# Performance work log

Hardware: AMD Instinct MI355X
Metric: run time of the kernel (lower is better)

The kernel has to match this reference:

```python
import jax, jax.numpy as jnp
import numpy as np

DIM = 192
HEADS = 6
WS = 7          # window size
SS = 3          # shift size
MLP_H = int(DIM * 4.0)
EPS_LN = 1e-5


def _static_tables():
    # Swin-v2 log-spaced continuous relative coords table: (1, 2*WS-1, 2*WS-1, 2)
    ch = np.arange(-(WS - 1), WS, dtype=np.float32)
    cw = np.arange(-(WS - 1), WS, dtype=np.float32)
    t = np.stack(np.meshgrid(ch, cw, indexing='ij'), axis=-1)[None]
    t[..., 0] /= (WS - 1)
    t[..., 1] /= (WS - 1)
    t *= 7.0
    t = np.sign(t) * np.log2(np.abs(t) + 1.0) / np.log2(7.0)
    # relative position index: (WS*WS, WS*WS)
    coords = np.stack(np.meshgrid(np.arange(WS), np.arange(WS), indexing='ij'))
    cf = coords.reshape(2, -1)
    rc = (cf[:, :, None] - cf[:, None, :]).transpose(1, 2, 0)
    rc[..., 0] += WS - 1
    rc[..., 1] += WS - 1
    rc[..., 0] *= 2 * WS - 1
    rpi = rc.sum(-1)
    return jnp.asarray(t, jnp.float32), jnp.asarray(rpi, jnp.int32)


def _attn_mask(H, W):
    # shifted-window mask: (nW, N, N) with 0 / -100
    img = np.zeros((H, W), np.float32)
    cnt = 0
    for hs in (slice(0, -WS), slice(-WS, -SS), slice(-SS, None)):
        for ws in (slice(0, -WS), slice(-WS, -SS), slice(-SS, None)):
            img[hs, ws] = cnt
            cnt += 1
    mw = img.reshape(H // WS, WS, W // WS, WS).transpose(0, 2, 1, 3).reshape(-1, WS * WS)
    am = mw[:, None, :] - mw[:, :, None]
    am = np.where(am != 0, -100.0, 0.0).astype(np.float32)
    return jnp.asarray(am)


def _ln(x, w, b):
    m = x.mean(-1, keepdims=True)
    v = ((x - m) ** 2).mean(-1, keepdims=True)
    return (x - m) / jnp.sqrt(v + EPS_LN) * w + b


def setup_inputs() -> dict:
    key = jax.random.key(0)
    ks = jax.random.split(key, 16)
    d = DIM
    inp = {
        'x': jax.random.normal(ks[0], (32, 56, 56, d), jnp.float32),
        'qkv_w': jax.random.normal(ks[1], (3 * d, d), jnp.float32) * (2.0 / d) ** 0.5,
        'qkv_b': jnp.full((3 * d,), 0.01, jnp.float32),
        'proj_w': jax.random.normal(ks[2], (d, d), jnp.float32) * (2.0 / d) ** 0.5,
        'proj_b': jnp.full((d,), 0.01, jnp.float32),
        'logit_scale': jnp.log(10.0 * jnp.ones((HEADS, 1, 1), jnp.float32)),
        'cpb_w1': jax.random.normal(ks[3], (512, 2), jnp.float32) * (2.0 / 2) ** 0.5,
        'cpb_b1': jnp.full((512,), 0.01, jnp.float32),
        'cpb_w2': jax.random.normal(ks[4], (HEADS, 512), jnp.float32) * (2.0 / 512) ** 0.5,
        'norm1_w': jnp.ones((d,), jnp.float32),
        'norm1_b': jnp.zeros((d,), jnp.float32),
        'norm2_w': jnp.ones((d,), jnp.float32),
        'norm2_b': jnp.zeros((d,), jnp.float32),
        'fc1_w': jax.random.normal(ks[5], (MLP_H, d), jnp.float32) * (2.0 / d) ** 0.5,
        'fc1_b': jnp.full((MLP_H,), 0.01, jnp.float32),
        'fc2_w': jax.random.normal(ks[6], (d, MLP_H), jnp.float32) * (2.0 / MLP_H) ** 0.5,
        'fc2_b': jnp.full((d,), 0.01, jnp.float32),
    }
    return inp


def reference(x, qkv_w, qkv_b, proj_w, proj_b, logit_scale, cpb_w1, cpb_b1, cpb_w2,
              norm1_w, norm1_b, norm2_w, norm2_b, fc1_w, fc1_b, fc2_w, fc2_b):
    B, H, W, C = x.shape
    N = WS * WS
    hd = C // HEADS
    table, rpi = _static_tables()
    mask = _attn_mask(H, W)  # (nW, N, N)
    nW = mask.shape[0]

    shortcut = x
    # cyclic shift + window partition: (B*nW, N, C)
    xs = jnp.roll(x, (-SS, -SS), axis=(1, 2))
    xw = xs.reshape(B, H // WS, WS, W // WS, WS, C).transpose(0, 1, 3, 2, 4, 5).reshape(-1, N, C)

    qkv = xw @ qkv_w.T + qkv_b
    qkv = qkv.reshape(-1, N, 3, HEADS, hd).transpose(2, 0, 3, 1, 4)
    q, k, v = qkv[0], qkv[1], qkv[2]  # (B_, H, N, hd)

    qn = q / jnp.clip(jnp.linalg.norm(q, axis=-1, keepdims=True), 1e-12)
    kn = k / jnp.clip(jnp.linalg.norm(k, axis=-1, keepdims=True), 1e-12)
    scale = jnp.exp(jnp.minimum(logit_scale, jnp.log(100.0)))  # (HEADS,1,1)
    attn = jnp.einsum('bhnd,bhmd->bhnm', qn, kn) * scale

    # CPB-MLP relative position bias
    hbt = jax.nn.leaky_relu(table @ cpb_w1.T + cpb_b1, 0.01) @ cpb_w2.T  # (1,13,13,HEADS)
    bias_table = hbt.reshape(-1, HEADS)
    rpb = bias_table[rpi.reshape(-1)].reshape(N, N, HEADS).transpose(2, 0, 1)
    attn = attn + (14.0 * jax.nn.sigmoid(rpb))[None]

    # shifted-window mask + softmax
    attn = attn.reshape(B, nW, HEADS, N, N) + mask[None, :, None]
    attn = jax.nn.softmax(attn.reshape(-1, HEADS, N, N), axis=-1)

    out = jnp.einsum('bhnm,bhmd->bnhd', attn, v).reshape(-1, N, C)
    out = out @ proj_w.T + proj_b

    # window reverse + reverse shift
    out = out.reshape(B, H // WS, W // WS, WS, WS, C).transpose(0, 1, 3, 2, 4, 5).reshape(B, H, W, C)
    out = jnp.roll(out, (SS, SS), axis=(1, 2))

    # post-norm residuals (Swin-v2 style)
    x1 = shortcut + _ln(out, norm1_w, norm1_b)
    mlp = jax.nn.gelu(x1 @ fc1_w.T + fc1_b, approximate=False) @ fc2_w.T + fc2_b
    return x1 + _ln(mlp, norm2_w, norm2_b)
```

## Files before the change

### kernel.cpp

```cpp
#include <hip/hip_runtime.h>
#include <math.h>

#define CDIM 192
#define NHEADS 6
#define HDIM 32
#define WSZ 7
#define NTOK 49
#define SHIFT 3
#define HW 56
#define MLPH 768
#define NTOKENS 100352
#define QKS 576
#define XS 200
#define VTS 72
#define PPS 72
#define LS 196
#define QPS 72
#define AS2 200
#define HS2 200
#define OS2 196

typedef __attribute__((ext_vector_type(8))) short short8;
typedef __attribute__((ext_vector_type(4))) float floatx4;
typedef unsigned short ushort_t;
typedef unsigned int uint_t;

__device__ __forceinline__ ushort_t f2b(float f) {
  uint_t u = __float_as_uint(f);
  u = (u + 0x7FFFu + ((u >> 16) & 1u)) >> 16;
  return (ushort_t)u;
}

__device__ __forceinline__ float gelu_fast(float v) {
  float u2 = 1.5957691f * v * (1.0f + 0.044715f * v * v);
  float s = 1.0f / (1.0f + __expf(-u2));
  return v * s;
}

__global__ void prep_kernel(const float* __restrict__ fc1_w, const float* __restrict__ fc2_w,
                            const float* __restrict__ qkv_w, const float* __restrict__ proj_w,
                            ushort_t* __restrict__ w1b, ushort_t* __restrict__ w2b,
                            ushort_t* __restrict__ qwb, ushort_t* __restrict__ pwb) {
  int i = blockIdx.x * 256 + threadIdx.x;
  if (i < MLPH*CDIM) w1b[i] = f2b(fc1_w[i]);
  else if (i < 2*MLPH*CDIM) w2b[i - MLPH*CDIM] = f2b(fc2_w[i - MLPH*CDIM]);
  else if (i < 2*MLPH*CDIM + 3*CDIM*CDIM) qwb[i - 2*MLPH*CDIM] = f2b(qkv_w[i - 2*MLPH*CDIM]);
  else if (i < 2*MLPH*CDIM + 4*CDIM*CDIM)
    pwb[i - 2*MLPH*CDIM - 3*CDIM*CDIM] = f2b(proj_w[i - 2*MLPH*CDIM - 3*CDIM*CDIM]);
}

__global__ __launch_bounds__(256) void cpb1_kernel(const float* __restrict__ w1,
                                                   const float* __restrict__ b1,
                                                   const float* __restrict__ w2,
                                                   float* __restrict__ bt) {
  int wave = threadIdx.x >> 6, lane = threadIdx.x & 63;
  int e = blockIdx.x * 4 + wave;
  if (e >= 169) return;
  const float inv_log2_7 = 0.35620718710802217f;
  int a = e / 13, b = e % 13;
  float v0 = (float)(a - 6) * (7.0f / 6.0f);
  float v1 = (float)(b - 6) * (7.0f / 6.0f);
  float s0 = (v0 > 0.f) ? 1.f : ((v0 < 0.f) ? -1.f : 0.f);
  float s1 = (v1 > 0.f) ? 1.f : ((v1 < 0.f) ? -1.f : 0.f);
  v0 = s0 * log2f(fabsf(v0) + 1.0f) * inv_log2_7;
  v1 = s1 * log2f(fabsf(v1) + 1.0f) * inv_log2_7;
  float acc[NHEADS];
  #pragma unroll
  for (int h = 0; h < NHEADS; ++h) acc[h] = 0.f;
  #pragma unroll
  for (int j = 0; j < 8; ++j) {
    int k = lane + 64*j;
    float hv = v0 * w1[2*k] + v1 * w1[2*k+1] + b1[k];
    hv = (hv > 0.f) ? hv : 0.01f * hv;
    #pragma unroll
    for (int h = 0; h < NHEADS; ++h) acc[h] += hv * w2[h*512 + k];
  }
  #pragma unroll
  for (int m = 1; m < 64; m <<= 1)
    #pragma unroll
    for (int h = 0; h < NHEADS; ++h) acc[h] += __shfl_xor(acc[h], m, 64);
  if (lane == 0) {
    #pragma unroll
    for (int h = 0; h < NHEADS; ++h) bt[e*NHEADS + h] = acc[h];
  }
}

__global__ void cpb2_kernel(const float* __restrict__ bt, float* __restrict__ abias) {
  int e = blockIdx.x * 256 + threadIdx.x;
  if (e >= NHEADS*NTOK*NTOK) return;
  int h = e / (NTOK*NTOK);
  int r = e % (NTOK*NTOK);
  int i = r / NTOK, j = r % NTOK;
  int idx = (i/7 - j/7 + 6) * 13 + (i%7 - j%7 + 6);
  float v = bt[idx*NHEADS + h];
  abias[e] = 14.0f / (1.0f + __expf(-v));
}

__global__ __launch_bounds__(384) void qkv_kernel(
    const float* __restrict__ x, const ushort_t* __restrict__ qwb,
    const float* __restrict__ qkv_b, ushort_t* __restrict__ qkvg) {
  __shared__ __align__(16) ushort_t s_a[64*AS2];
  int tid = threadIdx.x;
  int lane = tid & 63;
  int h = tid >> 6;
  int l15 = lane & 15, quad = lane >> 4;
  size_t tbase = (size_t)blockIdx.x * 64;

  for (int e = tid; e < 64*48; e += 384) {
    int t = e / 48, cc = (e % 48) * 4;
    float4 v = *(const float4*)(x + (tbase + t)*CDIM + cc);
    uint_t p0 = (uint_t)f2b(v.x) | ((uint_t)f2b(v.y) << 16);
    uint_t p1 = (uint_t)f2b(v.z) | ((uint_t)f2b(v.w) << 16);
    *(uint_t*)&s_a[t*AS2 + cc]     = p0;
    *(uint_t*)&s_a[t*AS2 + cc + 2] = p1;
  }
  __syncthreads();

  floatx4 acc[6][4];
  #pragma unroll
  for (int nt = 0; nt < 6; ++nt)
    #pragma unroll
    for (int mt = 0; mt < 4; ++mt) acc[nt][mt] = (floatx4){0.f,0.f,0.f,0.f};
  #pragma unroll
  for (int kt = 0; kt < 6; ++kt) {
    short8 a[4];
    #pragma unroll
    for (int mt = 0; mt < 4; ++mt)
      a[mt] = *(const short8*)&s_a[(mt*16 + l15)*AS2 + kt*32 + quad*8];
    #pragma unroll
    for (int nt = 0; nt < 6; ++nt) {
      int o = (nt >> 1)*CDIM + h*HDIM + (nt & 1)*16 + l15;
      short8 b = *(const short8*)&qwb[(size_t)o*CDIM + kt*32 + quad*8];
      #pragma unroll
      for (int mt = 0; mt < 4; ++mt)
        acc[nt][mt] = __builtin_amdgcn_mfma_f32_16x16x32_bf16(a[mt], b, acc[nt][mt], 0, 0, 0);
    }
  }
  #pragma unroll
  for (int w2 = 0; w2 < 2; ++w2) {
    float b0 = qkv_b[w2*CDIM + h*HDIM + l15];
    float b1 = qkv_b[w2*CDIM + h*HDIM + 16 + l15];
    #pragma unroll
    for (int mt = 0; mt < 4; ++mt) {
      float vv[2][4], ss[4];
      #pragma unroll
      for (int r = 0; r < 4; ++r) {
        float t0 = acc[w2*2][mt][r] + b0;
        float t1 = acc[w2*2+1][mt][r] + b1;
        vv[0][r] = t0; vv[1][r] = t1;
        ss[r] = t0*t0 + t1*t1;
      }
      #pragma unroll
      for (int m = 1; m < 16; m <<= 1)
        #pragma unroll
        for (int r = 0; r < 4; ++r) ss[r] += __shfl_xor(ss[r], m, 64);
      #pragma unroll
      for (int r = 0; r < 4; ++r) {
        float inv = 1.0f / fmaxf(sqrtf(ss[r]), 1e-12f);
        size_t tok = tbase + mt*16 + quad*4 + r;
        qkvg[tok*QKS + w2*CDIM + h*HDIM + l15]      = f2b(vv[0][r] * inv);
        qkvg[tok*QKS + w2*CDIM + h*HDIM + 16 + l15] = f2b(vv[1][r] * inv);
      }
    }
  }
  {
    float b0 = qkv_b[2*CDIM + h*HDIM + l15];
    float b1 = qkv_b[2*CDIM + h*HDIM + 16 + l15];
    #pragma unroll
    for (int mt = 0; mt < 4; ++mt)
      #pragma unroll
      for (int r = 0; r < 4; ++r) {
        size_t tok = tbase + mt*16 + quad*4 + r;
        qkvg[tok*QKS + 2*CDIM + h*HDIM + l15]      = f2b(acc[4][mt][r] + b0);
        qkvg[tok*QKS + 2*CDIM + h*HDIM + 16 + l15] = f2b(acc[5][mt][r] + b1);
      }
  }
}

__global__ __launch_bounds__(512, 4) void attn_kernel(
    const float* __restrict__ x, const ushort_t* __restrict__ qkvg,
    const ushort_t* __restrict__ pwb, const float* __restrict__ proj_b,
    const float* __restrict__ logit_scale, const float* __restrict__ abias,
    const float* __restrict__ n1w, const float* __restrict__ n1b,
    float* __restrict__ outp) {
  __shared__ __align__(16) ushort_t sm[192*VTS + 128*PPS + 64*XS];
  ushort_t* s_vt = sm;
  ushort_t* s_P  = sm + 192*VTS;
  ushort_t* s_o  = s_P + 128*PPS;
  float*    s_ln = (float*)sm;
  __shared__ float s_mu[NTOK], s_rs[NTOK];
  __shared__ int s_id[64];

  int tid = threadIdx.x;
  int lane = tid & 63;
  int wave = tid >> 6;
  int wm = wave & 3, wh = wave >> 2;
  int l15 = lane & 15, quad = lane >> 4;
  int mrow0 = wm*16 + quad*4;
  int blk = blockIdx.x;
  int bimg = blk >> 6, wh_b = (blk >> 3) & 7, ww_b = blk & 7;
  int rbase = wh_b*WSZ, cbase = ww_b*WSZ;

  int ti_a = wm*16 + l15; ti_a = (ti_a < NTOK) ? ti_a : (NTOK-1);
  int ra = rbase + ti_a/7 + SHIFT; ra -= (ra >= HW) ? HW : 0;
  int ca = cbase + ti_a%7 + SHIFT; ca -= (ca >= HW) ? HW : 0;
  uint_t qrow = (uint_t)((bimg*HW + ra)*HW + ca) * QKS;
  uint_t krow[4];
  #pragma unroll
  for (int nt = 0; nt < 4; ++nt) {
    int tn = nt*16 + l15; tn = (tn < NTOK) ? tn : (NTOK-1);
    int r = rbase + tn/7 + SHIFT; r -= (r >= HW) ? HW : 0;
    int c = cbase + tn%7 + SHIFT; c -= (c >= HW) ? HW : 0;
    krow[nt] = (uint_t)((bimg*HW + r)*HW + c) * QKS + CDIM;
  }
  short8 aq[3];
  #pragma unroll
  for (int hh = 0; hh < 3; ++hh)
    aq[hh] = *(const short8*)&qkvg[(size_t)qrow + (wh*3+hh)*HDIM + quad*8];

  if (tid < NTOK) {
    int r = rbase + tid/7;
    int c = cbase + tid%7;
    int hid = (r < HW-WSZ) ? 0 : ((r < HW-SHIFT) ? 1 : 2);
    int wid = (c < HW-WSZ) ? 0 : ((c < HW-SHIFT) ? 1 : 2);
    s_id[tid] = hid*3 + wid;
  }

  for (int e = tid; e < 32*48; e += 512) {
    int tp = e & 31, dg = e >> 5;
    int t0 = 2*tp, t1 = t0 + 1;
    uint2 va = make_uint2(0u, 0u), vb = make_uint2(0u, 0u);
    if (t0 < NTOK) {
      int r = rbase + t0/7 + SHIFT; r -= (r >= HW) ? HW : 0;
      int c = cbase + t0%7 + SHIFT; c -= (c >= HW) ? HW : 0;
      va = *(const uint2*)&qkvg[((size_t)((bimg*HW + r)*HW + c))*QKS + 2*CDIM + dg*4];
    }
    if (t1 < NTOK) {
      int r = rbase + t1/7 + SHIFT; r -= (r >= HW) ? HW : 0;
      int c = cbase + t1%7 + SHIFT; c -= (c >= HW) ? HW : 0;
      vb = *(const uint2*)&qkvg[((size_t)((bimg*HW + r)*HW + c))*QKS + 2*CDIM + dg*4];
    }
    int d = dg*4;
    *(uint_t*)&s_vt[(d  )*VTS + t0] = (va.x & 0xFFFFu) | (vb.x << 16);
    *(uint_t*)&s_vt[(d+1)*VTS + t0] = (va.x >> 16) | (vb.x & 0xFFFF0000u);
    *(uint_t*)&s_vt[(d+2)*VTS + t0] = (va.y & 0xFFFFu) | (vb.y << 16);
    *(uint_t*)&s_vt[(d+3)*VTS + t0] = (va.y >> 16) | (vb.y & 0xFFFF0000u);
  }
  __syncthreads();

  ushort_t* sPh = s_P + wave*16*PPS;
  for (int hh = 0; hh < 3; ++hh) {
    int h = wh*3 + hh;
    short8 bk[4];
    #pragma unroll
    for (int nt = 0; nt < 4; ++nt)
      bk[nt] = *(const short8*)&qkvg[(size_t)krow[nt] + h*HDIM + quad*8];
    floatx4 sv[4];
    #pragma unroll
    for (int nt = 0; nt < 4; ++nt)
      sv[nt] = __builtin_amdgcn_mfma_f32_16x16x32_bf16(aq[hh], bk[nt], (floatx4){0.f,0.f,0.f,0.f}, 0, 0, 0);
    float sc = __expf(fminf(logit_scale[h], 4.6051702f));
    #pragma unroll
    for (int r = 0; r < 4; ++r) {
      int m_tok = mrow0 + r;
      int mi = (m_tok < NTOK) ? m_tok : (NTOK-1);
      float srow[4];
      float mx = -1e30f;
      #pragma unroll
      for (int nt = 0; nt < 4; ++nt) {
        int n = nt*16 + l15;
        int ni = (n < NTOK) ? n : (NTOK-1);
        float s = sv[nt][r]*sc + abias[(h*NTOK + mi)*NTOK + ni];
        if (s_id[mi] != s_id[ni]) s -= 100.f;
        if (n >= NTOK) s = -1e30f;
        srow[nt] = s;
        mx = fmaxf(mx, s);
      }
      #pragma unroll
      for (int m = 1; m < 16; m <<= 1) mx = fmaxf(mx, __shfl_xor(mx, m, 64));
      float p[4], sum = 0.f;
      #pragma unroll
      for (int nt = 0; nt < 4; ++nt) { p[nt] = __expf(srow[nt] - mx); sum += p[nt]; }
      #pragma unroll
      for (int m = 1; m < 16; m <<= 1) sum += __shfl_xor(sum, m, 64);
      float inv = 1.0f / sum;
      #pragma unroll
      for (int nt = 0; nt < 4; ++nt) {
        int n = nt*16 + l15;
        sPh[(quad*4 + r)*PPS + n] = (n < NTOK) ? f2b(p[nt]*inv) : (ushort_t)0;
      }
    }
    floatx4 ov[2];
    ov[0] = (floatx4){0.f,0.f,0.f,0.f}; ov[1] = (floatx4){0.f,0.f,0.f,0.f};
    #pragma unroll
    for (int kt = 0; kt < 2; ++kt) {
      short8 ap = *(const short8*)&sPh[l15*PPS + kt*32 + quad*8];
      #pragma unroll
      for (int dt = 0; dt < 2; ++dt) {
        short8 bv = *(const short8*)&s_vt[(h*HDIM + dt*16 + l15)*VTS + kt*32 + quad*8];
        ov[dt] = __builtin_amdgcn_mfma_f32_16x16x32_bf16(ap, bv, ov[dt], 0, 0, 0);
      }
    }
    #pragma unroll
    for (int dt = 0; dt < 2; ++dt)
      #pragma unroll
      for (int r = 0; r < 4; ++r)
        s_o[(mrow0 + r)*XS + h*HDIM + dt*16 + l15] = f2b(ov[dt][r]);
  }
  __syncthreads();

  short8 aof[6];
  #pragma unroll
  for (int kt = 0; kt < 6; ++kt)
    aof[kt] = *(const short8*)&s_o[(wm*16 + l15)*XS + kt*32 + quad*8];
  floatx4 pacc[6];
  #pragma unroll
  for (int j = 0; j < 6; ++j) pacc[j] = (floatx4){0.f,0.f,0.f,0.f};
  #pragma unroll
  for (int kt = 0; kt < 6; ++kt) {
    #pragma unroll
    for (int j = 0; j < 6; ++j) {
      int n = wh*96 + j*16 + l15;
      short8 b = *(const short8*)&pwb[(size_t)n*CDIM + kt*32 + quad*8];
      pacc[j] = __builtin_amdgcn_mfma_f32_16x16x32_bf16(aof[kt], b, pacc[j], 0, 0, 0);
    }
  }
  #pragma unroll
  for (int j = 0; j < 6; ++j) {
    int c = wh*96 + j*16 + l15;
    float pb = proj_b[c];
    #pragma unroll
    for (int r = 0; r < 4; ++r) {
      int m = mrow0 + r;
      if (m < NTOK) s_ln[m*LS + c] = pacc[j][r] + pb;
    }
  }
  __syncthreads();
  if (tid < NTOK) {
    const float4* row = (const float4*)(s_ln + tid*LS);
    float mu = 0.f;
    #pragma unroll 8
    for (int c = 0; c < 48; ++c) { float4 v = row[c]; mu += v.x+v.y+v.z+v.w; }
    mu *= (1.0f/CDIM);
    float var = 0.f;
    #pragma unroll 8
    for (int c = 0; c < 48; ++c) {
      float4 v = row[c];
      float a0=v.x-mu, a1=v.y-mu, a2=v.z-mu, a3=v.w-mu;
      var += a0*a0 + a1*a1 + a2*a2 + a3*a3;
    }
    var *= (1.0f/CDIM);
    s_mu[tid] = mu; s_rs[tid] = rsqrtf(var + 1e-5f);
  }
  __syncthreads();
  for (int e = tid; e < NTOK*48; e += 512) {
    int ti = e / 48, cc = (e % 48) * 4;
    int r = (rbase + ti/WSZ + SHIFT) % HW;
    int cl = (cbase + ti%WSZ + SHIFT) % HW;
    size_t g = (((size_t)bimg*HW + r)*HW + cl)*CDIM + cc;
    float4 xv = *(const float4*)(x + g);
    float4 wv = *(const float4*)(n1w + cc);
    float4 bv = *(const float4*)(n1b + cc);
    float mu = s_mu[ti], rs = s_rs[ti];
    float4 o;
    o.x = xv.x + (s_ln[ti*LS+cc  ] - mu)*rs*wv.x + bv.x;
    o.y = xv.y + (s_ln[ti*LS+cc+1] - mu)*rs*wv.y + bv.y;
    o.z = xv.z + (s_ln[ti*LS+cc+2] - mu)*rs*wv.z + bv.z;
    o.w = xv.w + (s_ln[ti*LS+cc+3] - mu)*rs*wv.w + bv.w;
    *(float4*)(outp + g) = o;
  }
}

__global__ __launch_bounds__(512, 4) void attn_fused(
    const float* __restrict__ x, const ushort_t* __restrict__ qwb,
    const float* __restrict__ qkv_b, const ushort_t* __restrict__ pwb,
    const float* __restrict__ proj_b, const float* __restrict__ logit_scale,
    const float* __restrict__ abias, const float* __restrict__ n1w,
    const float* __restrict__ n1b, float* __restrict__ outp) {
  __shared__ __align__(16) ushort_t sm[64*XS + 2*64*QPS + 64*VTS + 2*64*PPS];
  ushort_t* s_x  = sm;
  ushort_t* s_qn = s_x  + 64*XS;
  ushort_t* s_kn = s_qn + 64*QPS;
  ushort_t* s_vt = s_kn + 64*QPS;
  ushort_t* s_P  = s_vt + 64*VTS;
  ushort_t* s_o  = s_x;
  float*    s_ln = (float*)sm;
  __shared__ float s_mu[NTOK], s_rs[NTOK];
  __shared__ int s_id[NTOK];

  int tid = threadIdx.x;
  int lane = tid & 63;
  int wave = tid >> 6;
  int wm = wave & 3, wh = wave >> 2;
  int l15 = lane & 15, quad = lane >> 4;
  int mrow0 = wm*16 + quad*4;
  int blk = blockIdx.x;
  int bimg = blk >> 6, wh_b = (blk >> 3) & 7, ww_b = blk & 7;

  for (int e = tid; e < 64*48; e += 512) {
    int i = e / 48, cc = (e % 48) * 4;
    uint_t p0 = 0, p1 = 0;
    if (i < NTOK) {
      int r = (wh_b*WSZ + i/WSZ + SHIFT) % HW;
      int c = (ww_b*WSZ + i%WSZ + SHIFT) % HW;
      float4 v = *(const float4*)(x + (((size_t)bimg*HW + r)*HW + c)*CDIM + cc);
      p0 = (uint_t)f2b(v.x) | ((uint_t)f2b(v.y) << 16);
      p1 = (uint_t)f2b(v.z) | ((uint_t)f2b(v.w) << 16);
    }
    *(uint_t*)&s_x[i*XS + cc]     = p0;
    *(uint_t*)&s_x[i*XS + cc + 2] = p1;
  }
  if (tid < NTOK) {
    int r = wh_b*WSZ + tid/WSZ;
    int c = ww_b*WSZ + tid%WSZ;
    int hid = (r < HW-WSZ) ? 0 : ((r < HW-SHIFT) ? 1 : 2);
    int wid = (c < HW-WSZ) ? 0 : ((c < HW-SHIFT) ? 1 : 2);
    s_id[tid] = hid*3 + wid;
  }
  __syncthreads();

  short8 axf[6];
  #pragma unroll
  for (int kt = 0; kt < 6; ++kt)
    axf[kt] = *(const short8*)&s_x[(wm*16 + l15)*XS + kt*32 + quad*8];

  for (int g = 0; g < 3; ++g) {
    int h = g*2 + wh;
    floatx4 acc[6];
    #pragma unroll
    for (int nt = 0; nt < 6; ++nt) acc[nt] = (floatx4){0.f,0.f,0.f,0.f};
    #pragma unroll
    for (int kt = 0; kt < 6; ++kt) {
      short8 a = axf[kt];
      #pragma unroll
      for (int nt = 0; nt < 6; ++nt) {
        int o = (nt >> 1)*CDIM + h*HDIM + (nt & 1)*16 + l15;
        short8 b = *(const short8*)&qwb[(size_t)o*CDIM + kt*32 + quad*8];
        acc[nt] = __builtin_amdgcn_mfma_f32_16x16x32_bf16(a, b, acc[nt], 0, 0, 0);
      }
    }
    #pragma unroll
    for (int w2 = 0; w2 < 2; ++w2) {
      float vv[2][4], ss[4];
      #pragma unroll
      for (int r = 0; r < 4; ++r) ss[r] = 0.f;
      #pragma unroll
      for (int dt = 0; dt < 2; ++dt) {
        float bias = qkv_b[w2*CDIM + h*HDIM + dt*16 + l15];
        #pragma unroll
        for (int r = 0; r < 4; ++r) {
          float t = acc[w2*2 + dt][r] + bias;
          vv[dt][r] = t; ss[r] += t*t;
        }
      }
      #pragma unroll
      for (int m = 1; m < 16; m <<= 1)
        #pragma unroll
        for (int r = 0; r < 4; ++r) ss[r] += __shfl_xor(ss[r], m, 64);
      ushort_t* dst = w2 ? s_kn : s_qn;
      #pragma unroll
      for (int r = 0; r < 4; ++r) {
        float inv = 1.0f / fmaxf(sqrtf(ss[r]), 1e-12f);
        #pragma unroll
        for (int dt = 0; dt < 2; ++dt)
          dst[(mrow0 + r)*QPS + wh*HDIM + dt*16 + l15] = f2b(vv[dt][r] * inv);
      }
    }
    #pragma unroll
    for (int dt = 0; dt < 2; ++dt) {
      float bias = qkv_b[2*CDIM + h*HDIM + dt*16 + l15];
      int d = wh*HDIM + dt*16 + l15;
      #pragma unroll
      for (int rp = 0; rp < 2; ++rp) {
        uint_t pk = (uint_t)f2b(acc[4+dt][2*rp] + bias) |
                    ((uint_t)f2b(acc[4+dt][2*rp+1] + bias) << 16);
        *(uint_t*)&s_vt[d*VTS + mrow0 + 2*rp] = pk;
      }
    }
    __syncthreads();

    short8 aq = *(const short8*)&s_qn[(wm*16 + l15)*QPS + wh*HDIM + quad*8];
    floatx4 sv[4];
    #pragma unroll
    for (int nt = 0; nt < 4; ++nt) {
      short8 bk = *(const short8*)&s_kn[(nt*16 + l15)*QPS + wh*HDIM + quad*8];
      sv[nt] = __builtin_amdgcn_mfma_f32_16x16x32_bf16(aq, bk, (floatx4){0.f,0.f,0.f,0.f}, 0, 0, 0);
    }
    float sc = __expf(fminf(logit_scale[h], 4.6051702f));
    ushort_t* sPh = s_P + wh*64*PPS;
    #pragma unroll
    for (int r = 0; r < 4; ++r) {
      int m_tok = mrow0 + r;
      int mi = (m_tok < NTOK) ? m_tok : (NTOK-1);
      float srow[4];
      float mx = -1e30f;
      #pragma unroll
      for (int nt = 0; nt < 4; ++nt) {
        int n = nt*16 + l15;
        int ni = (n < NTOK) ? n : (NTOK-1);
        float s = sv[nt][r]*sc + abias[(h*NTOK + mi)*NTOK + ni];
        if (s_id[mi] != s_id[ni]) s -= 100.f;
        if (n >= NTOK) s = -1e30f;
        srow[nt] = s;
        mx = fmaxf(mx, s);
      }
      #pragma unroll
      for (int m = 1; m < 16; m <<= 1) mx = fmaxf(mx, __shfl_xor(mx, m, 64));
      float p[4], sum = 0.f;
      #pragma unroll
      for (int nt = 0; nt < 4; ++nt) { p[nt] = __expf(srow[nt] - mx); sum += p[nt]; }
      #pragma unroll
      for (int m = 1; m < 16; m <<= 1) sum += __shfl_xor(sum, m, 64);
      float inv = 1.0f / sum;
      #pragma unroll
      for (int nt = 0; nt < 4; ++nt) {
        int n = nt*16 + l15;
        sPh[(mrow0 + r)*PPS + n] = (n < NTOK) ? f2b(p[nt]*inv) : (ushort_t)0;
      }
    }
    floatx4 ov[2];
    ov[0] = (floatx4){0.f,0.f,0.f,0.f}; ov[1] = (floatx4){0.f,0.f,0.f,0.f};
    #pragma unroll
    for (int kt = 0; kt < 2; ++kt) {
      short8 ap = *(const short8*)&sPh[(wm*16 + l15)*PPS + kt*32 + quad*8];
      #pragma unroll
      for (int dt = 0; dt < 2; ++dt) {
        short8 bv = *(const short8*)&s_vt[(wh*HDIM + dt*16 + l15)*VTS + kt*32 + quad*8];
        ov[dt] = __builtin_amdgcn_mfma_f32_16x16x32_bf16(ap, bv, ov[dt], 0, 0, 0);
      }
    }
    #pragma unroll
    for (int dt = 0; dt < 2; ++dt)
      #pragma unroll
      for (int r = 0; r < 4; ++r)
        s_o[(mrow0 + r)*XS + h*HDIM + dt*16 + l15] = f2b(ov[dt][r]);
    __syncthreads();
  }

  short8 aof[6];
  #pragma unroll
  for (int kt = 0; kt < 6; ++kt)
    aof[kt] = *(const short8*)&s_o[(wm*16 + l15)*XS + kt*32 + quad*8];
  __syncthreads();
  floatx4 pacc[6];
  #pragma unroll
  for (int j = 0; j < 6; ++j) pacc[j] = (floatx4){0.f,0.f,0.f,0.f};
  #pragma unroll
  for (int kt = 0; kt < 6; ++kt) {
    #pragma unroll
    for (int j = 0; j < 6; ++j) {
      int n = wh*96 + j*16 + l15;
      short8 b = *(const short8*)&pwb[(size_t)n*CDIM + kt*32 + quad*8];
      pacc[j] = __builtin_amdgcn_mfma_f32_16x16x32_bf16(aof[kt], b, pacc[j], 0, 0, 0);
    }
  }
  #pragma unroll
  for (int j = 0; j < 6; ++j) {
    int c = wh*96 + j*16 + l15;
    float pb = proj_b[c];
    #pragma unroll
    for (int r = 0; r < 4; ++r) {
      int m = mrow0 + r;
      if (m < NTOK) s_ln[m*LS + c] = pacc[j][r] + pb;
    }
  }
  __syncthreads();
  if (tid < NTOK) {
    const float4* row = (const float4*)(s_ln + tid*LS);
    float mu = 0.f;
    #pragma unroll 8
    for (int c = 0; c < 48; ++c) { float4 v = row[c]; mu += v.x+v.y+v.z+v.w; }
    mu *= (1.0f/CDIM);
    float var = 0.f;
    #pragma unroll 8
    for (int c = 0; c < 48; ++c) {
      float4 v = row[c];
      float a0=v.x-mu, a1=v.y-mu, a2=v.z-mu, a3=v.w-mu;
      var += a0*a0 + a1*a1 + a2*a2 + a3*a3;
    }
    var *= (1.0f/CDIM);
    s_mu[tid] = mu; s_rs[tid] = rsqrtf(var + 1e-5f);
  }
  __syncthreads();
  for (int e = tid; e < NTOK*48; e += 512) {
    int ti = e / 48, cc = (e % 48) * 4;
    int r = (wh_b*WSZ + ti/WSZ + SHIFT) % HW;
    int cl = (ww_b*WSZ + ti%WSZ + SHIFT) % HW;
    size_t g = (((size_t)bimg*HW + r)*HW + cl)*CDIM + cc;
    float4 xv = *(const float4*)(x + g);
    float4 wv = *(const float4*)(n1w + cc);
    float4 bv = *(const float4*)(n1b + cc);
    float mu = s_mu[ti], rs = s_rs[ti];
    float4 o;
    o.x = xv.x + (s_ln[ti*LS+cc  ] - mu)*rs*wv.x + bv.x;
    o.y = xv.y + (s_ln[ti*LS+cc+1] - mu)*rs*wv.y + bv.y;
    o.z = xv.z + (s_ln[ti*LS+cc+2] - mu)*rs*wv.z + bv.z;
    o.w = xv.w + (s_ln[ti*LS+cc+3] - mu)*rs*wv.w + bv.w;
    *(float4*)(outp + g) = o;
  }
}

__global__ __launch_bounds__(256) void mlp_kernel(
    const ushort_t* __restrict__ w1b, const ushort_t* __restrict__ w2b,
    const float* __restrict__ fc1_b, const float* __restrict__ fc2_b,
    const float* __restrict__ n2w, const float* __restrict__ n2b,
    float* __restrict__ io) {
  __shared__ __align__(16) ushort_t sm2[64*AS2 + 64*HS2];
  ushort_t* s_a = sm2;
  ushort_t* s_h = sm2 + 64*AS2;
  float*    s_o = (float*)sm2;
  __shared__ float s_mu[64], s_rs[64];

  int tid = threadIdx.x;
  int lane = tid & 63;
  int wave = tid >> 6;
  int l15 = lane & 15, quad = lane >> 4;
  size_t base = (size_t)blockIdx.x * (64*CDIM);

  for (int e = tid; e < 64*48; e += 256) {
    int t = e / 48, cc = (e % 48) * 4;
    float4 v = *(const float4*)(io + base + t*CDIM + cc);
    uint_t p0 = (uint_t)f2b(v.x) | ((uint_t)f2b(v.y) << 16);
    uint_t p1 = (uint_t)f2b(v.z) | ((uint_t)f2b(v.w) << 16);
    *(uint_t*)&s_a[t*AS2 + cc]     = p0;
    *(uint_t*)&s_a[t*AS2 + cc + 2] = p1;
  }
  __syncthreads();

  floatx4 oacc[12];
  #pragma unroll
  for (int t = 0; t < 12; ++t) oacc[t] = (floatx4){0.f,0.f,0.f,0.f};

  for (int ch = 0; ch < 4; ++ch) {
    floatx4 hacc[12];
    #pragma unroll
    for (int t = 0; t < 12; ++t) hacc[t] = (floatx4){0.f,0.f,0.f,0.f};
    #pragma unroll
    for (int kt = 0; kt < 6; ++kt) {
      short8 a[4];
      #pragma unroll
      for (int mt = 0; mt < 4; ++mt)
        a[mt] = *(const short8*)&s_a[(mt*16 + l15)*AS2 + kt*32 + quad*8];
      #pragma unroll
      for (int nt = 0; nt < 3; ++nt) {
        int n = ch*192 + wave*48 + nt*16 + l15;
        short8 b = *(const short8*)&w1b[(size_t)n*CDIM + kt*32 + quad*8];
        #pragma unroll
        for (int mt = 0; mt < 4; ++mt)
          hacc[nt*4+mt] = __builtin_amdgcn_mfma_f32_16x16x32_bf16(a[mt], b, hacc[nt*4+mt], 0, 0, 0);
      }
    }
    #pragma unroll
    for (int nt = 0; nt < 3; ++nt) {
      int n = ch*192 + wave*48 + nt*16 + l15;
      int cloc = wave*48 + nt*16 + l15;
      float bias = fc1_b[n];
      #pragma unroll
      for (int mt = 0; mt < 4; ++mt) {
        #pragma unroll
        for (int r = 0; r < 4; ++r) {
          float v = hacc[nt*4+mt][r] + bias;
          s_h[(mt*16 + quad*4 + r)*HS2 + cloc] = f2b(gelu_fast(v));
        }
      }
    }
    __syncthreads();
    #pragma unroll
    for (int kt = 0; kt < 6; ++kt) {
      short8 a2[4];
      #pragma unroll
      for (int mt = 0; mt < 4; ++mt)
        a2[mt] = *(const short8*)&s_h[(mt*16 + l15)*HS2 + kt*32 + quad*8];
      #pragma unroll
      for (int nt = 0; nt < 3; ++nt) {
        int n2 = wave*48 + nt*16 + l15;
        short8 b2 = *(const short8*)&w2b[(size_t)n2*MLPH + ch*192 + kt*32 + quad*8];
        #pragma unroll
        for (int mt = 0; mt < 4; ++mt)
          oacc[nt*4+mt] = __builtin_amdgcn_mfma_f32_16x16x32_bf16(a2[mt], b2, oacc[nt*4+mt], 0, 0, 0);
      }
    }
    __syncthreads();
  }

  #pragma unroll
  for (int nt = 0; nt < 3; ++nt) {
    int c = wave*48 + nt*16 + l15;
    float bb = fc2_b[c];
    #pragma unroll
    for (int mt = 0; mt < 4; ++mt) {
      #pragma unroll
      for (int r = 0; r < 4; ++r)
        s_o[(mt*16 + quad*4 + r)*OS2 + c] = oacc[nt*4+mt][r] + bb;
    }
  }
  __syncthreads();
  if (tid < 64) {
    const float4* row = (const float4*)(s_o + tid*OS2);
    float mu = 0.f;
    #pragma unroll 8
    for (int c = 0; c < 48; ++c) { float4 v = row[c]; mu += v.x+v.y+v.z+v.w; }
    mu *= (1.0f/CDIM);
    float var = 0.f;
    #pragma unroll 8
    for (int c = 0; c < 48; ++c) {
      float4 v = row[c];
      float a0=v.x-mu, a1=v.y-mu, a2=v.z-mu, a3=v.w-mu;
      var += a0*a0 + a1*a1 + a2*a2 + a3*a3;
    }
    var *= (1.0f/CDIM);
    s_mu[tid] = mu; s_rs[tid] = rsqrtf(var + 1e-5f);
  }
  __syncthreads();
  for (int e = tid; e < 64*48; e += 256) {
    int t = e / 48, cc = (e % 48) * 4;
    float4 xv = *(const float4*)(io + base + t*CDIM + cc);
    float4 wv = *(const float4*)(n2w + cc);
    float4 bv = *(const float4*)(n2b + cc);
    float mu = s_mu[t], rs = s_rs[t];
    float4 o;
    o.x = xv.x + (s_o[t*OS2+cc  ] - mu)*rs*wv.x + bv.x;
    o.y = xv.y + (s_o[t*OS2+cc+1] - mu)*rs*wv.y + bv.y;
    o.z = xv.z + (s_o[t*OS2+cc+2] - mu)*rs*wv.z + bv.z;
    o.w = xv.w + (s_o[t*OS2+cc+3] - mu)*rs*wv.w + bv.w;
    *(float4*)(io + base + t*CDIM + cc) = o;
  }
}

extern "C" void kernel_launch(void* const* d_in, const int* in_sizes, int n_in,
                              void* d_out, int out_size, void* d_ws, size_t ws_size,
                              hipStream_t stream) {
  const float* x           = (const float*)d_in[0];
  const float* qkv_w       = (const float*)d_in[1];
  const float* qkv_b       = (const float*)d_in[2];
  const float* proj_w      = (const float*)d_in[3];
  const float* proj_b      = (const float*)d_in[4];
  const float* logit_scale = (const float*)d_in[5];
  const float* cpb_w1      = (const float*)d_in[6];
  const float* cpb_b1      = (const float*)d_in[7];
  const float* cpb_w2      = (const float*)d_in[8];
  const float* n1w         = (const float*)d_in[9];
  const float* n1b         = (const float*)d_in[10];
  const float* n2w         = (const float*)d_in[11];
  const float* n2b         = (const float*)d_in[12];
  const float* fc1_w       = (const float*)d_in[13];
  const float* fc1_b       = (const float*)d_in[14];
  const float* fc2_w       = (const float*)d_in[15];
  const float* fc2_b       = (const float*)d_in[16];
  float* out = (float*)d_out;

  ushort_t* w1b = (ushort_t*)d_ws;
  ushort_t* w2b = w1b + MLPH*CDIM;
  ushort_t* qwb = w2b + CDIM*MLPH;
  ushort_t* pwb = qwb + 3*CDIM*CDIM;
  float* abias  = (float*)(pwb + CDIM*CDIM);
  float* bt     = abias + NHEADS*NTOK*NTOK;
  ushort_t* qkvg = (ushort_t*)(bt + 169*NHEADS);

  size_t base_b = (size_t)(2*MLPH*CDIM + 4*CDIM*CDIM)*2
                + (size_t)(NHEADS*NTOK*NTOK)*4 + (size_t)(169*NHEADS)*4;
  size_t qkvg_b = (size_t)NTOKENS*QKS*2;
  bool split_qkv = ws_size >= base_b + qkvg_b;

  int prep_elems = 2*MLPH*CDIM + 4*CDIM*CDIM;
  hipLaunchKernelGGL(prep_kernel, dim3((prep_elems + 255)/256), dim3(256), 0, stream,
                     fc1_w, fc2_w, qkv_w, proj_w, w1b, w2b, qwb, pwb);
  hipLaunchKernelGGL(cpb1_kernel, dim3((169 + 3)/4), dim3(256), 0, stream,
                     cpb_w1, cpb_b1, cpb_w2, bt);
  hipLaunchKernelGGL(cpb2_kernel, dim3((NHEADS*NTOK*NTOK + 255)/256), dim3(256), 0, stream,
                     bt, abias);
  if (split_qkv) {
    hipLaunchKernelGGL(qkv_kernel, dim3(NTOKENS/64), dim3(384), 0, stream,
                       x, qwb, qkv_b, qkvg);
    hipLaunchKernelGGL(attn_kernel, dim3(2048), dim3(512), 0, stream,
                       x, qkvg, pwb, proj_b, logit_scale, abias, n1w, n1b, out);
  } else {
    hipLaunchKernelGGL(attn_fused, dim3(2048), dim3(512), 0, stream,
                       x, qwb, qkv_b, pwb, proj_b, logit_scale, abias, n1w, n1b, out);
  }
  hipLaunchKernelGGL(mlp_kernel, dim3(NTOKENS/64), dim3(256), 0, stream,
                     w1b, w2b, fc1_b, fc2_b, n2w, n2b, out);
}
```

Before: 631.6 us.

## Precombine shift mask into bias table, double-buffer MLP hidden, use native bf16 cast

The shifted-window mask is folded into four precomputed bias tables, one per window-boundary class, so the attention kernels read a single combined bias and drop the shared-memory id lookup and compare. The MLP kernel ping-pongs between two hidden-activation buffers, which lets it drop one barrier per chunk at the cost of extra LDS. The float-to-bf16 conversion uses the compiler's native cast in place of manual rounding. The cost is a larger bias table and higher LDS use in the MLP kernel, which may lower occupancy.

```diff
diff --git a/kernel.cpp b/kernel.cpp
--- a/kernel.cpp
+++ b/kernel.cpp
@@ -26,9 +26,8 @@
 typedef unsigned int uint_t;
 
 __device__ __forceinline__ ushort_t f2b(float f) {
-  uint_t u = __float_as_uint(f);
-  u = (u + 0x7FFFu + ((u >> 16) & 1u)) >> 16;
-  return (ushort_t)u;
+  __bf16 b = (__bf16)f;
+  return __builtin_bit_cast(ushort_t, b);
 }
 
 __device__ __forceinline__ float gelu_fast(float v) {
@@ -85,15 +84,26 @@
   }
 }
 
-__global__ void cpb2_kernel(const float* __restrict__ bt, float* __restrict__ abias) {
+__global__ void cpb2_kernel(const float* __restrict__ bt, float* __restrict__ cbias) {
   int e = blockIdx.x * 256 + threadIdx.x;
-  if (e >= NHEADS*NTOK*NTOK) return;
-  int h = e / (NTOK*NTOK);
-  int r = e % (NTOK*NTOK);
+  if (e >= 4*NHEADS*NTOK*NTOK) return;
+  int cls = e / (NHEADS*NTOK*NTOK);
+  int rem = e % (NHEADS*NTOK*NTOK);
+  int h = rem / (NTOK*NTOK);
+  int r = rem % (NTOK*NTOK);
   int i = r / NTOK, j = r % NTOK;
   int idx = (i/7 - j/7 + 6) * 13 + (i%7 - j%7 + 6);
   float v = bt[idx*NHEADS + h];
-  abias[e] = 14.0f / (1.0f + __expf(-v));
+  float b = 14.0f / (1.0f + __expf(-v));
+  int clsh = cls >> 1, clsw = cls & 1;
+  int ri = (clsh ? HW-WSZ : 0) + i/7, rj = (clsh ? HW-WSZ : 0) + j/7;
+  int ci = (clsw ? HW-WSZ : 0) + i%7, cj = (clsw ? HW-WSZ : 0) + j%7;
+  int hi = (ri < HW-WSZ) ? 0 : ((ri < HW-SHIFT) ? 1 : 2);
+  int hj = (rj < HW-WSZ) ? 0 : ((rj < HW-SHIFT) ? 1 : 2);
+  int wi = (ci < HW-WSZ) ? 0 : ((ci < HW-SHIFT) ? 1 : 2);
+  int wj = (cj < HW-WSZ) ? 0 : ((cj < HW-SHIFT) ? 1 : 2);
+  if ((hi*3 + wi) != (hj*3 + wj)) b -= 100.f;
+  cbias[e] = b;
 }
 
 __global__ __launch_bounds__(384) void qkv_kernel(
@@ -180,7 +190,7 @@
 __global__ __launch_bounds__(512, 4) void attn_kernel(
     const float* __restrict__ x, const ushort_t* __restrict__ qkvg,
     const ushort_t* __restrict__ pwb, const float* __restrict__ proj_b,
-    const float* __restrict__ logit_scale, const float* __restrict__ abias,
+    const float* __restrict__ logit_scale, const float* __restrict__ cbias,
     const float* __restrict__ n1w, const float* __restrict__ n1b,
     float* __restrict__ outp) {
   __shared__ __align__(16) ushort_t sm[192*VTS + 128*PPS + 64*XS];
@@ -189,7 +199,6 @@
   ushort_t* s_o  = s_P + 128*PPS;
   float*    s_ln = (float*)sm;
   __shared__ float s_mu[NTOK], s_rs[NTOK];
-  __shared__ int s_id[64];
 
   int tid = threadIdx.x;
   int lane = tid & 63;
@@ -200,6 +209,8 @@
   int blk = blockIdx.x;
   int bimg = blk >> 6, wh_b = (blk >> 3) & 7, ww_b = blk & 7;
   int rbase = wh_b*WSZ, cbase = ww_b*WSZ;
+  const float* cb = cbias +
+      (size_t)(((wh_b == 7) ? 2 : 0) + ((ww_b == 7) ? 1 : 0)) * (NHEADS*NTOK*NTOK);
 
   int ti_a = wm*16 + l15; ti_a = (ti_a < NTOK) ? ti_a : (NTOK-1);
   int ra = rbase + ti_a/7 + SHIFT; ra -= (ra >= HW) ? HW : 0;
@@ -217,14 +228,6 @@
   #pragma unroll
   for (int hh = 0; hh < 3; ++hh)
     aq[hh] = *(const short8*)&qkvg[(size_t)qrow + (wh*3+hh)*HDIM + quad*8];
-
-  if (tid < NTOK) {
-    int r = rbase + tid/7;
-    int c = cbase + tid%7;
-    int hid = (r < HW-WSZ) ? 0 : ((r < HW-SHIFT) ? 1 : 2);
-    int wid = (c < HW-WSZ) ? 0 : ((c < HW-SHIFT) ? 1 : 2);
-    s_id[tid] = hid*3 + wid;
-  }
 
   for (int e = tid; e < 32*48; e += 512) {
     int tp = e & 31, dg = e >> 5;
@@ -270,8 +273,7 @@
       for (int nt = 0; nt < 4; ++nt) {
         int n = nt*16 + l15;
         int ni = (n < NTOK) ? n : (NTOK-1);
-        float s = sv[nt][r]*sc + abias[(h*NTOK + mi)*NTOK + ni];
-        if (s_id[mi] != s_id[ni]) s -= 100.f;
+        float s = sv[nt][r]*sc + cb[(h*NTOK + mi)*NTOK + ni];
         if (n >= NTOK) s = -1e30f;
         srow[nt] = s;
         mx = fmaxf(mx, s);
@@ -375,7 +377,7 @@
     const float* __restrict__ x, const ushort_t* __restrict__ qwb,
     const float* __restrict__ qkv_b, const ushort_t* __restrict__ pwb,
     const float* __restrict__ proj_b, const float* __restrict__ logit_scale,
-    const float* __restrict__ abias, const float* __restrict__ n1w,
+    const float* __restrict__ cbias, const float* __restrict__ n1w,
     const float* __restrict__ n1b, float* __restrict__ outp) {
   __shared__ __align__(16) ushort_t sm[64*XS + 2*64*QPS + 64*VTS + 2*64*PPS];
   ushort_t* s_x  = sm;
@@ -386,7 +388,6 @@
   ushort_t* s_o  = s_x;
   float*    s_ln = (float*)sm;
   __shared__ float s_mu[NTOK], s_rs[NTOK];
-  __shared__ int s_id[NTOK];
 
   int tid = threadIdx.x;
   int lane = tid & 63;
@@ -396,6 +397,8 @@
   int mrow0 = wm*16 + quad*4;
   int blk = blockIdx.x;
   int bimg = blk >> 6, wh_b = (blk >> 3) & 7, ww_b = blk & 7;
+  const float* cb = cbias +
+      (size_t)(((wh_b == 7) ? 2 : 0) + ((ww_b == 7) ? 1 : 0)) * (NHEADS*NTOK*NTOK);
 
   for (int e = tid; e < 64*48; e += 512) {
     int i = e / 48, cc = (e % 48) * 4;
@@ -410,13 +413,6 @@
     *(uint_t*)&s_x[i*XS + cc]     = p0;
     *(uint_t*)&s_x[i*XS + cc + 2] = p1;
   }
-  if (tid < NTOK) {
-    int r = wh_b*WSZ + tid/WSZ;
-    int c = ww_b*WSZ + tid%WSZ;
-    int hid = (r < HW-WSZ) ? 0 : ((r < HW-SHIFT) ? 1 : 2);
-    int wid = (c < HW-WSZ) ? 0 : ((c < HW-SHIFT) ? 1 : 2);
-    s_id[tid] = hid*3 + wid;
-  }
   __syncthreads();
 
   short8 axf[6];
@@ -498,8 +494,7 @@
       for (int nt = 0; nt < 4; ++nt) {
         int n = nt*16 + l15;
         int ni = (n < NTOK) ? n : (NTOK-1);
-        float s = sv[nt][r]*sc + abias[(h*NTOK + mi)*NTOK + ni];
-        if (s_id[mi] != s_id[ni]) s -= 100.f;
+        float s = sv[nt][r]*sc + cb[(h*NTOK + mi)*NTOK + ni];
         if (n >= NTOK) s = -1e30f;
         srow[nt] = s;
         mx = fmaxf(mx, s);
@@ -605,10 +600,11 @@
     const float* __restrict__ fc1_b, const float* __restrict__ fc2_b,
     const float* __restrict__ n2w, const float* __restrict__ n2b,
     float* __restrict__ io) {
-  __shared__ __align__(16) ushort_t sm2[64*AS2 + 64*HS2];
-  ushort_t* s_a = sm2;
-  ushort_t* s_h = sm2 + 64*AS2;
-  float*    s_o = (float*)sm2;
+  __shared__ __align__(16) ushort_t sm2[64*AS2 + 2*64*HS2];
+  ushort_t* s_a  = sm2;
+  ushort_t* s_h0 = sm2 + 64*AS2;
+  ushort_t* s_h1 = s_h0 + 64*HS2;
+  float*    s_o  = (float*)sm2;
   __shared__ float s_mu[64], s_rs[64];
 
   int tid = threadIdx.x;
@@ -631,7 +627,9 @@
   #pragma unroll
   for (int t = 0; t < 12; ++t) oacc[t] = (floatx4){0.f,0.f,0.f,0.f};
 
+  #pragma unroll
   for (int ch = 0; ch < 4; ++ch) {
+    ushort_t* sh = (ch & 1) ? s_h1 : s_h0;
     floatx4 hacc[12];
     #pragma unroll
     for (int t = 0; t < 12; ++t) hacc[t] = (floatx4){0.f,0.f,0.f,0.f};
@@ -660,7 +658,7 @@
         #pragma unroll
         for (int r = 0; r < 4; ++r) {
           float v = hacc[nt*4+mt][r] + bias;
-          s_h[(mt*16 + quad*4 + r)*HS2 + cloc] = f2b(gelu_fast(v));
+          sh[(mt*16 + quad*4 + r)*HS2 + cloc] = f2b(gelu_fast(v));
         }
       }
     }
@@ -670,7 +668,7 @@
       short8 a2[4];
       #pragma unroll
       for (int mt = 0; mt < 4; ++mt)
-        a2[mt] = *(const short8*)&s_h[(mt*16 + l15)*HS2 + kt*32 + quad*8];
+        a2[mt] = *(const short8*)&sh[(mt*16 + l15)*HS2 + kt*32 + quad*8];
       #pragma unroll
       for (int nt = 0; nt < 3; ++nt) {
         int n2 = wave*48 + nt*16 + l15;
@@ -680,7 +678,6 @@
           oacc[nt*4+mt] = __builtin_amdgcn_mfma_f32_16x16x32_bf16(a2[mt], b2, oacc[nt*4+mt], 0, 0, 0);
       }
     }
-    __syncthreads();
   }
 
   #pragma unroll
@@ -753,12 +750,12 @@
   ushort_t* w2b = w1b + MLPH*CDIM;
   ushort_t* qwb = w2b + CDIM*MLPH;
   ushort_t* pwb = qwb + 3*CDIM*CDIM;
-  float* abias  = (float*)(pwb + CDIM*CDIM);
-  float* bt     = abias + NHEADS*NTOK*NTOK;
+  float* cbias  = (float*)(pwb + CDIM*CDIM);
+  float* bt     = cbias + 4*NHEADS*NTOK*NTOK;
   ushort_t* qkvg = (ushort_t*)(bt + 169*NHEADS);
 
   size_t base_b = (size_t)(2*MLPH*CDIM + 4*CDIM*CDIM)*2
-                + (size_t)(NHEADS*NTOK*NTOK)*4 + (size_t)(169*NHEADS)*4;
+                + (size_t)(4*NHEADS*NTOK*NTOK)*4 + (size_t)(169*NHEADS)*4;
   size_t qkvg_b = (size_t)NTOKENS*QKS*2;
   bool split_qkv = ws_size >= base_b + qkvg_b;
 
@@ -767,16 +764,16 @@
                      fc1_w, fc2_w, qkv_w, proj_w, w1b, w2b, qwb, pwb);
   hipLaunchKernelGGL(cpb1_kernel, dim3((169 + 3)/4), dim3(256), 0, stream,
                      cpb_w1, cpb_b1, cpb_w2, bt);
-  hipLaunchKernelGGL(cpb2_kernel, dim3((NHEADS*NTOK*NTOK + 255)/256), dim3(256), 0, stream,
-                     bt, abias);
+  hipLaunchKernelGGL(cpb2_kernel, dim3((4*NHEADS*NTOK*NTOK + 255)/256), dim3(256), 0, stream,
+                     bt, cbias);
   if (split_qkv) {
     hipLaunchKernelGGL(qkv_kernel, dim3(NTOKENS/64), dim3(384), 0, stream,
                        x, qwb, qkv_b, qkvg);
     hipLaunchKernelGGL(attn_kernel, dim3(2048), dim3(512), 0, stream,
-                       x, qkvg, pwb, proj_b, logit_scale, abias, n1w, n1b, out);
+                       x, qkvg, pwb, proj_b, logit_scale, cbias, n1w, n1b, out);
   } else {
     hipLaunchKernelGGL(attn_fused, dim3(2048), dim3(512), 0, stream,
-                       x, qwb, qkv_b, pwb, proj_b, logit_scale, abias, n1w, n1b, out);
+                       x, qwb, qkv_b, pwb, proj_b, logit_scale, cbias, n1w, n1b, out);
   }
   hipLaunchKernelGGL(mlp_kernel, dim3(NTOKENS/64), dim3(256), 0, stream,
                      w1b, w2b, fc1_b, fc2_b, n2w, n2b, out);
```

After: 593.0 us. 1.07x faster.
